# Performance work log

Hardware: AMD Instinct MI355X
Metric: run time of the kernel (lower is better)

Reference implementation:

```python
import jax, jax.numpy as jnp
import numpy as np

B, L, C = 4, 2052, 1024
H, D = 16, 64          # num_heads, head_dim
NREG = 4               # register tokens, bypass RoPE
LN_EPS = 1e-5


def setup_inputs() -> dict:
    key = jax.random.key(0)
    ks = jax.random.split(key, 6)
    s = 1.0 / np.sqrt(C)
    return {
        "x": jax.random.normal(ks[0], (B, L, C), jnp.float32),
        "rope_embed": jax.random.normal(ks[1], (2, L - NREG, D), jnp.float32),  # [cos; sin]
        "Wqkv": jax.random.normal(ks[2], (C, 3 * C), jnp.float32) * s,
        "bqkv": jnp.zeros((3 * C,), jnp.float32),
        "Wproj": jax.random.normal(ks[3], (C, C), jnp.float32) * s,
        "bproj": jnp.zeros((C,), jnp.float32),
        "ln_gamma": jnp.ones((C,), jnp.float32),
        "ln_beta": jnp.zeros((C,), jnp.float32),
    }


def _rotate_half(x):
    x1, x2 = jnp.split(x, 2, axis=-1)
    return jnp.concatenate([-x2, x1], axis=-1)


def _apply_rope(q, k, rope_embed, n_reg):
    # q,k: (B,H,L,D); rope_embed: (2, L-n_reg, D)
    cos = rope_embed[0][None, None]  # (1,1,Ls,D)
    sin = rope_embed[1][None, None]
    def rot(t):
        reg, sp = t[:, :, :n_reg], t[:, :, n_reg:]
        sp = sp * cos + _rotate_half(sp) * sin
        return jnp.concatenate([reg, sp], axis=2)
    return rot(q), rot(k)


def reference(x, rope_embed, Wqkv, bqkv, Wproj, bproj, ln_gamma, ln_beta):
    # QKV projection: (B,L,3C) -> (3,B,H,L,D)
    qkv = (x @ Wqkv + bqkv).reshape(B, L, 3, H, D).transpose(2, 0, 3, 1, 4)
    q, k, v = qkv[0], qkv[1], qkv[2]
    q, k = _apply_rope(q, k, rope_embed, NREG)
    # SDPA (no dropout, not causal)
    scale = 1.0 / np.sqrt(D)
    logits = jnp.einsum("bhqd,bhkd->bhqk", q, k) * scale
    attn = jax.nn.softmax(logits, axis=-1)
    out = jnp.einsum("bhqk,bhkd->bhqd", attn, v)
    out = out.transpose(0, 2, 1, 3).reshape(B, L, C)
    # post-attention LayerNorm
    mu = jnp.mean(out, axis=-1, keepdims=True)
    var = jnp.mean(jnp.square(out - mu), axis=-1, keepdims=True)
    out = (out - mu) * jax.lax.rsqrt(var + LN_EPS) * ln_gamma + ln_beta
    # output projection
    return out @ Wproj + bproj
```

## Files before the change

### kernel.cpp

```cpp
#include <hip/hip_runtime.h>
#include <hip/hip_bf16.h>

#define B_ 4
#define L_ 2052
#define C_ 1024
#define H_ 16
#define D_ 64
#define NREG_ 4
#define M_ (B_*L_)
#define LP_ 2056
#define QSC 0.18033688f

typedef short bf16x8 __attribute__((ext_vector_type(8)));
typedef float f32x4 __attribute__((ext_vector_type(4)));
typedef __hip_bfloat16 bf16;

#define MFMA(a,b,c) __builtin_amdgcn_mfma_f32_16x16x32_bf16(a,b,c,0,0,0)

__device__ inline float b2f(bf16 v){ return __bfloat162float(v); }
__device__ inline bf16  f2b(float v){ return __float2bfloat16(v); }
__device__ inline bf16x8 as8(int4 v){ union{int4 i; bf16x8 b;} u; u.i=v; return u.b; }

__device__ inline void gl_lds16(const void* g, void* l){
    __builtin_amdgcn_global_load_lds(
        (const __attribute__((address_space(1))) void*)g,
        (__attribute__((address_space(3))) void*)l,
        16, 0, 0);
}

__device__ inline int xcd_swizzle(int orig, int nwg){
    int xcd = orig & 7, idx = orig >> 3;
    int q8 = nwg >> 3, r8 = nwg & 7;
    return (xcd < r8 ? xcd*(q8+1) : r8*(q8+1) + (xcd-r8)*q8) + idx;
}

__global__ __launch_bounds__(256)
void cvt_split(const float* __restrict__ in, bf16* __restrict__ hi,
               bf16* __restrict__ lo, int n)
{
    int i = (blockIdx.x*256 + threadIdx.x)*4;
    if (i >= n) return;
    float4 v = *(const float4*)(in + i);
    int2 hraw, lraw;
    bf16* hp = (bf16*)&hraw;
    bf16* lp = (bf16*)&lraw;
    float vv[4] = {v.x, v.y, v.z, v.w};
    #pragma unroll
    for (int j=0;j<4;++j){
        bf16 h = f2b(vv[j]);
        hp[j] = h;
        lp[j] = f2b(vv[j] - b2f(h));
    }
    *(int2*)(hi + i) = hraw;
    *(int2*)(lo + i) = lraw;
}

__global__ __launch_bounds__(256)
void transpose_cvt(const float* __restrict__ in, bf16* __restrict__ out,
                   int R, int Cc)
{
    __shared__ bf16 t[32][33];
    int bx = blockIdx.x * 32;
    int by = blockIdx.y * 32;
    int tx = threadIdx.x;
    int ty = threadIdx.y;
    #pragma unroll
    for (int i=0;i<4;++i){
        int r = by + ty + i*8;
        int c = bx + tx;
        t[ty+i*8][tx] = f2b(in[(size_t)r*Cc + c]);
    }
    __syncthreads();
    #pragma unroll
    for (int i=0;i<4;++i){
        int r = bx + ty + i*8;
        int c = by + tx;
        out[(size_t)r*R + c] = t[tx][ty+i*8];
    }
}

template<typename OutT, bool SPLIT, bool ROPE>
__global__ __launch_bounds__(256,2)
void gemm_wide(const bf16* __restrict__ A, const bf16* __restrict__ Alo,
               const bf16* __restrict__ Bt, const float* __restrict__ bias,
               const float* __restrict__ rope_t,
               OutT* __restrict__ C, int M, int N, int K, int NBX)
{
    __shared__ bf16 As[128*32];
    __shared__ bf16 Als[SPLIT ? 128*32 : 8];
    __shared__ bf16 Bs[256*32];

    int tid  = threadIdx.x;
    int lane = tid & 63, wave = tid >> 6;
    int wm = (wave>>1)*64, wn = (wave&1)*128;
    int wg = xcd_swizzle(blockIdx.x, gridDim.x);
    int bm = (wg / NBX)*128, bn = (wg % NBX)*256;
    int lrow = lane & 15;
    int quad = lane >> 4;
    int sw8  = (quad ^ ((lrow>>2)&3)) * 8;

    f32x4 acc[4][8] = {};

    for (int k0 = 0; k0 < K; k0 += 32) {
        #pragma unroll
        for (int it=0; it<2; ++it) {
            int o  = (wave*2+it)*1024 + lane*16;
            int r  = o >> 6;
            int p  = (o >> 4) & 3;
            int ls = p ^ ((r>>2)&3);
            int ga = bm + r; if (ga >= M) ga = M-1;
            gl_lds16(A + (size_t)ga*K + k0 + ls*8, &As[(wave*2+it)*512]);
            if constexpr (SPLIT)
                gl_lds16(Alo + (size_t)ga*K + k0 + ls*8, &Als[(wave*2+it)*512]);
        }
        #pragma unroll
        for (int it=0; it<4; ++it) {
            int o  = (wave*4+it)*1024 + lane*16;
            int r  = o >> 6;
            int p  = (o >> 4) & 3;
            int ls = p ^ ((r>>2)&3);
            gl_lds16(Bt + (size_t)(bn + r)*K + k0 + ls*8, &Bs[(wave*4+it)*512]);
        }
        __syncthreads();

        bf16x8 b[8];
        #pragma unroll
        for (int i=0;i<8;++i)
            b[i] = *(const bf16x8*)(&Bs[(wn+i*16+lrow)*32 + sw8]);
        #pragma unroll
        for (int mi=0;mi<4;++mi){
            bf16x8 a = *(const bf16x8*)(&As[(wm+mi*16+lrow)*32 + sw8]);
            #pragma unroll
            for (int ni=0;ni<8;++ni)
                acc[mi][ni] = MFMA(a, b[ni], acc[mi][ni]);
            if constexpr (SPLIT) {
                bf16x8 al = *(const bf16x8*)(&Als[(wm+mi*16+lrow)*32 + sw8]);
                #pragma unroll
                for (int ni=0;ni<8;++ni)
                    acc[mi][ni] = MFMA(al, b[ni], acc[mi][ni]);
            }
        }
        __syncthreads();
    }

    float bv[8];
    #pragma unroll
    for (int ni=0;ni<8;++ni) bv[ni] = bias[bn + wn + ni*16 + lrow];

    if constexpr (ROPE) {
        int region = (bn + wn) >> 10;
        #pragma unroll
        for (int mi=0;mi<4;++mi){
            #pragma unroll
            for (int r=0;r<4;++r){
                int row = bm + wm + mi*16 + quad*4 + r;
                if (row >= M) continue;
                int l = row % L_;
                float vv[8];
                #pragma unroll
                for (int ni=0;ni<8;++ni) vv[ni] = acc[mi][ni][r] + bv[ni];
                if (region < 2 && l >= NREG_){
                    const float* cp = rope_t + (size_t)(l - NREG_)*D_;
                    const float* sp = rope_t + (size_t)(L_ - NREG_)*D_ + (size_t)(l - NREG_)*D_;
                    #pragma unroll
                    for (int pi=0; pi<4; ++pi){
                        int n0 = (pi&1) + (pi>>1)*4;
                        int n1 = n0 + 2;
                        int d  = (pi&1)*16 + lrow;
                        float a = vv[n0], b2 = vv[n1];
                        vv[n0] = a*cp[d]      - b2*sp[d];
                        vv[n1] = b2*cp[d+32]  + a*sp[d+32];
                    }
                }
                #pragma unroll
                for (int ni=0;ni<8;++ni)
                    C[(size_t)row*N + bn + wn + ni*16 + lrow] = f2b(vv[ni]);
            }
        }
    } else {
        #pragma unroll
        for (int ni=0;ni<8;++ni){
            int col = bn + wn + ni*16 + lrow;
            #pragma unroll
            for (int mi=0;mi<4;++mi){
                int rowb = bm + wm + mi*16 + quad*4;
                #pragma unroll
                for (int r=0;r<4;++r){
                    int row = rowb + r;
                    if (row < M) {
                        float v = acc[mi][ni][r] + bv[ni];
                        if constexpr (sizeof(OutT)==4) C[(size_t)row*N + col] = v;
                        else                           C[(size_t)row*N + col] = f2b(v);
                    }
                }
            }
        }
    }
}

__global__ __launch_bounds__(256)
void transpose_v(const bf16* __restrict__ qkv, bf16* __restrict__ Vt)
{
    __shared__ bf16 t[64*72];
    int bh = blockIdx.y, lt = blockIdx.x;
    int b = bh >> 4, h = bh & 15;
    int tid = threadIdx.x;
    #pragma unroll
    for (int it=0; it<2; ++it){
        int i = tid + it*256;
        int il = i >> 3, c = (i&7)*8;
        int l = lt*64 + il;
        int4 v = {0,0,0,0};
        if (l < L_) v = *(const int4*)(qkv + ((size_t)b*L_ + l)*3072 + 2048 + h*64 + c);
        *(int4*)(&t[il*72 + c]) = v;
    }
    __syncthreads();
    #pragma unroll
    for (int it=0; it<2; ++it){
        int i = tid + it*256;
        int d = i >> 3, ck = (i&7)*8;
        if (lt*64 + ck + 8 <= LP_){
            union { int4 q; bf16 e[8]; } u;
            #pragma unroll
            for (int j=0;j<8;++j) u.e[j] = t[(ck+j)*72 + d];
            *(int4*)(&Vt[((size_t)bh*64 + d)*LP_ + lt*64 + ck]) = u.q;
        }
    }
}

__global__ __launch_bounds__(256,3)
void attn_kernel(const bf16* __restrict__ qkv, const bf16* __restrict__ Vt,
                 float* __restrict__ out)
{
    __shared__ bf16 sK[64*64];
    __shared__ bf16 sV[64*64];

    int tid = threadIdx.x, lane = tid & 63, wave = tid >> 6;
    int lrow = lane & 15, quad = lane >> 4;
    int wg = xcd_swizzle(blockIdx.x, gridDim.x);
    int qt = wg % 11, bh = wg / 11;
    int b  = bh >> 4, h = bh & 15;
    size_t rowbase = (size_t)b * L_;
    int q0 = qt * 192;

    int l8   = lane >> 3;
    int p3   = lane & 7;
    int swz0 = (quad     ^ (lrow&7))*8;
    int swz1 = ((4+quad) ^ (lrow&7))*8;

    bf16x8 qf[3][2];
    #pragma unroll
    for (int qi=0;qi<3;++qi){
        int gq = q0 + wave*48 + qi*16 + lrow;
        if (gq >= L_) gq = L_-1;
        const bf16* qp = qkv + (rowbase + gq)*3072 + h*64 + quad*8;
        qf[qi][0] = *(const bf16x8*)(qp);
        qf[qi][1] = *(const bf16x8*)(qp + 32);
    }

    f32x4 o_[3][4] = {};
    f32x4 lsum[3] = {};

    bf16x8 onesf;
    #pragma unroll
    for (int j=0;j<8;++j) onesf[j] = (short)0x3F80;

    const bf16* kgbase = qkv + rowbase*3072 + 1024 + h*64;
    const bf16* vgbase = Vt + (size_t)bh*64*LP_;

    for (int kt = 0; kt <= 32; ++kt) {
        #pragma unroll
        for (int it=0; it<2; ++it){
            int ci  = wave*2 + it;
            int row = ci*8 + l8;
            int ls  = p3 ^ (row&7);
            int key = kt*64 + ((row & 0x23) | ((row & 0x0C) << 1) | ((row & 0x10) >> 2));
            if (key >= L_) key = L_-1;
            gl_lds16(kgbase + (size_t)key*3072 + ls*8, &sK[ci*512]);
        }
        #pragma unroll
        for (int it=0; it<2; ++it){
            int ci  = wave*2 + it;
            int row = ci*8 + l8;
            int ls  = p3 ^ (row&7);
            int col = kt*64 + ls*8;
            if (col + 8 > LP_) col = 0;
            gl_lds16(vgbase + (size_t)row*LP_ + col, &sV[ci*512]);
        }
        __syncthreads();

        bool full = (kt != 32);
        int4 pb[3][2];

        #pragma unroll
        for (int ki=0; ki<4; ++ki){
            bf16x8 kf0 = *(const bf16x8*)(&sK[(ki*16+lrow)*64 + swz0]);
            bf16x8 kf1 = *(const bf16x8*)(&sK[(ki*16+lrow)*64 + swz1]);
            #pragma unroll
            for (int qi=0; qi<3; ++qi){
                f32x4 t = {};
                t = MFMA(kf0, qf[qi][0], t);
                t = MFMA(kf1, qf[qi][1], t);
                float p[4];
                #pragma unroll
                for (int r=0;r<4;++r){
                    float e = __builtin_amdgcn_exp2f(t[r]*QSC);
                    int keyi = (ki>>1)*32 + quad*8 + (ki&1)*4 + r;
                    p[r] = (full || (2048 + keyi) < L_) ? e : 0.f;
                }
                union { int2 d2; __hip_bfloat162 h2[2]; } u;
                u.h2[0] = __float22bfloat162_rn({p[0], p[1]});
                u.h2[1] = __float22bfloat162_rn({p[2], p[3]});
                if ((ki & 1) == 0){ pb[qi][ki>>1].x = u.d2.x; pb[qi][ki>>1].y = u.d2.y; }
                else              { pb[qi][ki>>1].z = u.d2.x; pb[qi][ki>>1].w = u.d2.y; }
            }
        }

        #pragma unroll
        for (int ni=0; ni<4; ++ni){
            bf16x8 vf0 = *(const bf16x8*)(&sV[(ni*16+lrow)*64 + swz0]);
            bf16x8 vf1 = *(const bf16x8*)(&sV[(ni*16+lrow)*64 + swz1]);
            #pragma unroll
            for (int mi=0; mi<3; ++mi){
                f32x4 t = o_[mi][ni];
                t = MFMA(vf0, as8(pb[mi][0]), t);
                t = MFMA(vf1, as8(pb[mi][1]), t);
                o_[mi][ni] = t;
            }
        }
        #pragma unroll
        for (int mi=0; mi<3; ++mi){
            lsum[mi] = MFMA(onesf, as8(pb[mi][0]), lsum[mi]);
            lsum[mi] = MFMA(onesf, as8(pb[mi][1]), lsum[mi]);
        }
        __syncthreads();
    }

    #pragma unroll
    for (int mi=0; mi<3; ++mi){
        float inv = 1.f / lsum[mi][0];
        int lq = q0 + wave*48 + mi*16 + lrow;
        if (lq < L_){
            size_t base = (rowbase + lq)*1024 + h*64;
            #pragma unroll
            for (int ni=0; ni<4; ++ni){
                f32x4 t = o_[mi][ni];
                float4 w = {t[0]*inv, t[1]*inv, t[2]*inv, t[3]*inv};
                *(float4*)(&out[base + ni*16 + quad*4]) = w;
            }
        }
    }
}

__global__ __launch_bounds__(256)
void ln_kernel(const float* __restrict__ in, const float* __restrict__ gamma,
               const float* __restrict__ beta, bf16* __restrict__ y)
{
    int row = blockIdx.x;
    int tid = threadIdx.x;
    int wave = tid >> 6, lane = tid & 63;
    float4 v4 = *(const float4*)(in + (size_t)row*1024 + tid*4);
    float v[4] = {v4.x, v4.y, v4.z, v4.w};
    float s = 0.f, q = 0.f;
    #pragma unroll
    for (int j=0;j<4;++j){ s += v[j]; q += v[j]*v[j]; }
    #pragma unroll
    for (int o=1;o<64;o<<=1){ s += __shfl_xor(s, o); q += __shfl_xor(q, o); }
    __shared__ float sh[8];
    if (lane == 0){ sh[wave] = s; sh[4+wave] = q; }
    __syncthreads();
    s = sh[0]+sh[1]+sh[2]+sh[3];
    q = sh[4]+sh[5]+sh[6]+sh[7];
    float mu  = s * (1.f/1024.f);
    float var = q * (1.f/1024.f) - mu*mu;
    float rstd = rsqrtf(var + 1e-5f);
    int2 raw;
    bf16* ob = (bf16*)&raw;
    #pragma unroll
    for (int j=0;j<4;++j){
        float g = gamma[tid*4+j], be = beta[tid*4+j];
        ob[j] = f2b((v[j]-mu)*rstd*g + be);
    }
    *(int2*)(y + (size_t)row*1024 + tid*4) = raw;
}

extern "C" void kernel_launch(void* const* d_in, const int* in_sizes, int n_in,
                              void* d_out, int out_size, void* d_ws, size_t ws_size,
                              hipStream_t stream)
{
    const float* x     = (const float*)d_in[0];
    const float* rope  = (const float*)d_in[1];
    const float* Wqkv  = (const float*)d_in[2];
    const float* bqkv  = (const float*)d_in[3];
    const float* Wproj = (const float*)d_in[4];
    const float* bproj = (const float*)d_in[5];
    const float* lng   = (const float*)d_in[6];
    const float* lnb   = (const float*)d_in[7];
    float* out = (float*)d_out;

    char* ws = (char*)d_ws;
    size_t off = 0;
    auto alloc = [&](size_t bytes)->char* {
        char* p = ws + off;
        off += (bytes + 255) & ~(size_t)255;
        return p;
    };
    bf16* xhi    = (bf16*)alloc((size_t)M_*C_*2);
    bf16* xlo    = (bf16*)alloc((size_t)M_*C_*2);
    bf16* WqkvT  = (bf16*)alloc((size_t)3*C_*C_*2);
    bf16* WprojT = (bf16*)alloc((size_t)C_*C_*2);
    bf16* qkv    = (bf16*)alloc((size_t)M_*3*C_*2);
    bf16* Vt     = (bf16*)alloc((size_t)B_*H_*D_*LP_*2);

    float* attnF = (float*)xhi;
    bf16*  y     = qkv;

    cvt_split<<<M_*C_/1024, 256, 0, stream>>>(x, xhi, xlo, M_*C_);
    transpose_cvt<<<dim3(3*C_/32, C_/32), dim3(32,8), 0, stream>>>(Wqkv, WqkvT, C_, 3*C_);
    transpose_cvt<<<dim3(C_/32, C_/32), dim3(32,8), 0, stream>>>(Wproj, WprojT, C_, C_);
    gemm_wide<bf16, true, true><<<(3*C_/256)*((M_+127)/128), 256, 0, stream>>>(
        xhi, xlo, WqkvT, bqkv, rope, qkv, M_, 3*C_, C_, 3*C_/256);
    transpose_v<<<dim3((L_+63)/64, B_*H_), 256, 0, stream>>>(qkv, Vt);
    attn_kernel<<<((L_+191)/192)*B_*H_, 256, 0, stream>>>(qkv, Vt, attnF);
    ln_kernel<<<M_, 256, 0, stream>>>(attnF, lng, lnb, y);
    gemm_wide<float, false, false><<<(C_/256)*((M_+127)/128), 256, 0, stream>>>(
        y, nullptr, WprojT, bproj, nullptr, out, M_, C_, C_, C_/256);
}
```

Measured before the change: 384.6 us.

## Double-buffer LDS tiles in wide GEMM to overlap global loads with MFMA

Adds a second LDS buffer for the A, A-lo and B tiles so the next K-slice is fetched with global_load_lds while the current slice feeds the MFMAs. Explicit vmcnt waits and raw s_barrier calls replace __syncthreads. The goal is to hide global-memory latency in the QKV and projection GEMMs. LDS use doubles, which may lower occupancy under launch_bounds(256,2). The hand-counted vmcnt values must exactly match the number of loads issued per stage.

```diff
diff --git a/kernel.cpp b/kernel.cpp
--- a/kernel.cpp
+++ b/kernel.cpp
@@ -86,9 +86,9 @@
                const float* __restrict__ rope_t,
                OutT* __restrict__ C, int M, int N, int K, int NBX)
 {
-    __shared__ bf16 As[128*32];
-    __shared__ bf16 Als[SPLIT ? 128*32 : 8];
-    __shared__ bf16 Bs[256*32];
+    __shared__ bf16 As[2][128*32];
+    __shared__ bf16 Als[SPLIT ? 2*128*32 : 8];
+    __shared__ bf16 Bs[2][256*32];
 
     int tid  = threadIdx.x;
     int lane = tid & 63, wave = tid >> 6;
@@ -101,7 +101,7 @@
 
     f32x4 acc[4][8] = {};
 
-    for (int k0 = 0; k0 < K; k0 += 32) {
+    auto STAGE = [&](int buf, int k0){
         #pragma unroll
         for (int it=0; it<2; ++it) {
             int o  = (wave*2+it)*1024 + lane*16;
@@ -109,9 +109,9 @@
             int p  = (o >> 4) & 3;
             int ls = p ^ ((r>>2)&3);
             int ga = bm + r; if (ga >= M) ga = M-1;
-            gl_lds16(A + (size_t)ga*K + k0 + ls*8, &As[(wave*2+it)*512]);
+            gl_lds16(A + (size_t)ga*K + k0 + ls*8, &As[buf][(wave*2+it)*512]);
             if constexpr (SPLIT)
-                gl_lds16(Alo + (size_t)ga*K + k0 + ls*8, &Als[(wave*2+it)*512]);
+                gl_lds16(Alo + (size_t)ga*K + k0 + ls*8, &Als[buf*4096 + (wave*2+it)*512]);
         }
         #pragma unroll
         for (int it=0; it<4; ++it) {
@@ -119,28 +119,43 @@
             int r  = o >> 6;
             int p  = (o >> 4) & 3;
             int ls = p ^ ((r>>2)&3);
-            gl_lds16(Bt + (size_t)(bn + r)*K + k0 + ls*8, &Bs[(wave*4+it)*512]);
-        }
-        __syncthreads();
+            gl_lds16(Bt + (size_t)(bn + r)*K + k0 + ls*8, &Bs[buf][(wave*4+it)*512]);
+        }
+    };
+
+    int nt = K >> 5;
+    int cur = 0;
+    STAGE(0, 0);
+
+    for (int t = 0; t < nt; ++t) {
+        if (t+1 < nt) {
+            STAGE(cur^1, (t+1)*32);
+            if constexpr (SPLIT) asm volatile("s_waitcnt vmcnt(8)" ::: "memory");
+            else                 asm volatile("s_waitcnt vmcnt(6)" ::: "memory");
+        } else {
+            asm volatile("s_waitcnt vmcnt(0)" ::: "memory");
+        }
+        __builtin_amdgcn_s_barrier();
 
         bf16x8 b[8];
         #pragma unroll
         for (int i=0;i<8;++i)
-            b[i] = *(const bf16x8*)(&Bs[(wn+i*16+lrow)*32 + sw8]);
+            b[i] = *(const bf16x8*)(&Bs[cur][(wn+i*16+lrow)*32 + sw8]);
         #pragma unroll
         for (int mi=0;mi<4;++mi){
-            bf16x8 a = *(const bf16x8*)(&As[(wm+mi*16+lrow)*32 + sw8]);
+            bf16x8 a = *(const bf16x8*)(&As[cur][(wm+mi*16+lrow)*32 + sw8]);
             #pragma unroll
             for (int ni=0;ni<8;++ni)
                 acc[mi][ni] = MFMA(a, b[ni], acc[mi][ni]);
             if constexpr (SPLIT) {
-                bf16x8 al = *(const bf16x8*)(&Als[(wm+mi*16+lrow)*32 + sw8]);
+                bf16x8 al = *(const bf16x8*)(&Als[cur*4096 + (wm+mi*16+lrow)*32 + sw8]);
                 #pragma unroll
                 for (int ni=0;ni<8;++ni)
                     acc[mi][ni] = MFMA(al, b[ni], acc[mi][ni]);
             }
         }
-        __syncthreads();
+        __builtin_amdgcn_s_barrier();
+        cur ^= 1;
     }
 
     float bv[8];
```

After: 384.4 us. No clear change (-0.0%).
